# Optimization experiments

Hardware: AMD Instinct MI355X
Metric: run time of the kernel (lower is better)

## Reference

```python
import jax, jax.numpy as jnp
import numpy as np

# Dims: B nodes, Z species (elements), IN/OUT channels, M = 2*l+1 (l=1)
B, Z, IN, OUT, M = 8192, 10, 512, 512, 3
ALPHA = 1.0 / np.sqrt(IN)  # self.alpha = 1/sqrt(in_dim)
SQRT3 = float(np.sqrt(3.0))


def setup_inputs() -> dict:
    key = jax.random.key(0)
    k1, k2, k3 = jax.random.split(key, 3)
    t = jax.random.normal(k1, (B, IN, M), dtype=jnp.float32)
    species = jax.random.randint(k2, (B,), 0, Z)
    node_attrs = jax.nn.one_hot(species, Z, dtype=jnp.float32)  # [B, Z] one-hot
    # torch.nn.init.uniform_(weights, -sqrt(3), sqrt(3))
    weights = jax.random.uniform(k3, (Z, OUT, IN), dtype=jnp.float32,
                                 minval=-SQRT3, maxval=SQRT3)
    return {"t": t, "node_attrs": node_attrs, "weights": weights}


def reference(t, node_attrs, weights):
    # Faithful to: einsum('bz, zCc, bcd -> bCd', node_attrs, weights*alpha, t)
    # Contract weights with t first per species ([Z,B,C,M], ~500MB), which
    # avoids the huge [B,C,c] per-node weight-gather intermediate, then
    # select/sum over species with the one-hot node_attrs.
    W = weights * ALPHA                       # [Z, OUT, IN]
    zt = jnp.einsum('zCc,bcd->zbCd', W, t)    # [Z, B, OUT, M]
    out = jnp.einsum('bz,zbCd->bCd', node_attrs, zt)  # [B, OUT, M]
    return out
```

## Files before the change

### kernel.cpp

```cpp
#include <hip/hip_runtime.h>
#include <stdint.h>

#define NB   8192
#define NZ   10
#define CIN  512
#define COUT 512
#define MM   3
#define ALPHA 0.04419417382415922f

#define ROWS_TOTAL (NB * MM)
#define BM 128
#define BN 128
#define BK 32
#define KITERS (CIN / BK)
#define MAX_MT (ROWS_TOTAL / BM + NZ)
#define NYB (COUT / BN)
#define NWG (MAX_MT * NYB)
#define NGRP 32

typedef short bf16x8 __attribute__((ext_vector_type(8)));
typedef float f32x4  __attribute__((ext_vector_type(4)));

__device__ __forceinline__ uint16_t f2bf(float f) {
    union { float f; uint32_t i; } v; v.f = f;
    uint32_t x = v.i;
    x += 0x7fffu + ((x >> 16) & 1u);
    return (uint16_t)(x >> 16);
}
__device__ __forceinline__ uint32_t pack2(float a, float b) {
    return (uint32_t)f2bf(a) | ((uint32_t)f2bf(b) << 16);
}
__device__ __forceinline__ void async16(const void* g, void* l) {
    __builtin_amdgcn_global_load_lds((const uint32_t*)g, (uint32_t*)l, 16, 0, 0);
}

__global__ __launch_bounds__(256)
void prep_kernel(const float* __restrict__ attrs, const float* __restrict__ w,
                 int* __restrict__ species, int* __restrict__ hist,
                 ushort* __restrict__ wt) {
    const int tid = threadIdx.x;
    if (blockIdx.x >= NGRP) {
        const size_t base = (size_t)(blockIdx.x - NGRP) * 2048;
        const float* src = w + base;
        ushort* dst = wt + base;
        float4 a = *(const float4*)(src + tid * 4);
        float4 b = *(const float4*)(src + 1024 + tid * 4);
        uint2 oa, ob;
        oa.x = pack2(a.x, a.y); oa.y = pack2(a.z, a.w);
        ob.x = pack2(b.x, b.y); ob.y = pack2(b.z, b.w);
        *(uint2*)(dst + tid * 4) = oa;
        *(uint2*)(dst + 1024 + tid * 4) = ob;
        return;
    }
    __shared__ int wc[4][NZ];
    const int b = blockIdx.x * 256 + tid;
    const float* a = attrs + (size_t)b * NZ;
    int s = 0;
    #pragma unroll
    for (int z = 0; z < NZ; z++) if (a[z] > 0.5f) s = z;
    species[b] = s;
    const int wv = tid >> 6, lane = tid & 63;
    #pragma unroll
    for (int z = 0; z < NZ; z++) {
        unsigned long long m = __ballot(s == z);
        if (lane == 0) wc[wv][z] = __popcll(m);
    }
    __syncthreads();
    if (tid < NZ) {
        hist[blockIdx.x * NZ + tid] = wc[0][tid] + wc[1][tid] + wc[2][tid] + wc[3][tid];
    }
}

__global__ __launch_bounds__(256)
void place_kernel(const int* __restrict__ species, const int* __restrict__ hist,
                  int* __restrict__ sorted, int* __restrict__ offsets,
                  int* __restrict__ tile_offsets) {
    __shared__ int lhist[NGRP][NZ];
    __shared__ int loff[NZ + 1], ltoff[NZ + 1];
    __shared__ int pb[NZ];
    __shared__ int wc[4][NZ];
    const int tid = threadIdx.x, g = blockIdx.x;

    for (int i = tid; i < NGRP * NZ; i += 256) ((int*)lhist)[i] = hist[i];
    __syncthreads();
    if (tid == 0) {
        int off = 0, toff = 0;
        for (int z = 0; z < NZ; z++) {
            int tot = 0;
            for (int gg = 0; gg < NGRP; gg++) tot += lhist[gg][z];
            loff[z] = off; ltoff[z] = toff;
            off += tot;
            toff += (3 * tot + BM - 1) / BM;
        }
        loff[NZ] = off; ltoff[NZ] = toff;
    }
    __syncthreads();
    if (tid < NZ) {
        int base = loff[tid];
        for (int gg = 0; gg < g; gg++) base += lhist[gg][tid];
        pb[tid] = base;
    }
    if (g == 0 && tid < NZ + 1) {
        offsets[tid] = loff[tid];
        tile_offsets[tid] = ltoff[tid];
    }
    const int b = g * 256 + tid;
    const int s = species[b];
    const int wv = tid >> 6, lane = tid & 63;
    unsigned long long mymask = 0;
    #pragma unroll
    for (int z = 0; z < NZ; z++) {
        unsigned long long m = __ballot(s == z);
        if (lane == 0) wc[wv][z] = __popcll(m);
        if (s == z) mymask = m;
    }
    __syncthreads();
    int rank = __popcll(mymask & ((1ull << lane) - 1ull));
    #pragma unroll
    for (int w2 = 0; w2 < 4; w2++) if (w2 < wv) rank += wc[w2][s];
    sorted[pb[s] + rank] = b;
}

__global__ __launch_bounds__(256)
void pack_t(const float* __restrict__ t, const int* __restrict__ sorted,
            ushort* __restrict__ tt) {
    const int w = threadIdx.x >> 6, L = threadIdx.x & 63;
    const int p = blockIdx.x * 4 + w;
    const int node = sorted[p];
    const float4* src = (const float4*)(t + (size_t)node * (CIN * MM) + L * 24);
    float4 f[6];
    #pragma unroll
    for (int i = 0; i < 6; i++) f[i] = src[i];
    const float* v = (const float*)f;
    #pragma unroll
    for (int d = 0; d < MM; d++) {
        uint4 o;
        o.x = pack2(v[d],      v[3 + d]);
        o.y = pack2(v[6 + d],  v[9 + d]);
        o.z = pack2(v[12 + d], v[15 + d]);
        o.w = pack2(v[18 + d], v[21 + d]);
        *(uint4*)&tt[(size_t)(3 * p + d) * CIN + L * 8] = o;
    }
}

__global__ __launch_bounds__(256)
void gemm_kernel(const ushort* __restrict__ tt, const ushort* __restrict__ wt,
                 const int* __restrict__ sorted, const int* __restrict__ offsets,
                 const int* __restrict__ tile_offsets, float* __restrict__ out) {
    __shared__ __align__(16) ushort smem[2][2][BM][BK];
    __shared__ int spos[48];

    const int bid = blockIdx.x;
    const int nid = (bid & 7) * (NWG / 8) + (bid >> 3);
    const int tz = nid >> 2;
    const int Cbase = (nid & 3) * BN;

    if (tz >= tile_offsets[NZ]) return;
    int z = 0;
    #pragma unroll
    for (int i = 1; i < NZ; i++) if (tile_offsets[i] <= tz) z = i;

    const int row_base = 3 * offsets[z] + (tz - tile_offsets[z]) * BM;
    const int row_end  = 3 * offsets[z + 1];
    const int pos0     = row_base / 3;

    const int tid = threadIdx.x;
    const int w = tid >> 6, L = tid & 63;
    if (tid < 48) spos[tid] = sorted[min(pos0 + tid, NB - 1)];

    const int lr = L >> 2;
    const int cs = (L & 3) ^ ((L >> 3) & 3);
    const int soff = lr * CIN + cs * 8;
    const ushort* gA = tt + (size_t)(row_base + w * 32) * CIN + soff;
    const ushort* gB = wt + ((size_t)z * COUT + Cbase + w * 32) * CIN + soff;

    const int wm = w & 1, wn = w >> 1;
    const int q = L >> 4, mr = L & 15;
    const int sr8 = (q ^ ((mr >> 1) & 3)) * 8;

    f32x4 acc[4][4];
    #pragma unroll
    for (int i = 0; i < 4; i++)
        #pragma unroll
        for (int j = 0; j < 4; j++) acc[i][j] = (f32x4){0.f, 0.f, 0.f, 0.f};

#define STAGE(bufi, ko) do {                                        \
        async16(gA + (ko),                  &smem[0][bufi][w * 32][0]);      \
        async16(gA + 16 * CIN + (ko),       &smem[0][bufi][w * 32 + 16][0]); \
        async16(gB + (ko),                  &smem[1][bufi][w * 32][0]);      \
        async16(gB + 16 * CIN + (ko),       &smem[1][bufi][w * 32 + 16][0]); \
    } while (0)

    STAGE(0, 0);
    for (int kt = 0; kt < KITERS; kt++) {
        const int cur = kt & 1;
        if (kt + 1 < KITERS) {
            STAGE(cur ^ 1, (kt + 1) * BK);
            asm volatile("s_waitcnt vmcnt(4)" ::: "memory");
        } else {
            asm volatile("s_waitcnt vmcnt(0)" ::: "memory");
        }
        asm volatile("s_barrier" ::: "memory");

        bf16x8 af[4], bf[4];
        #pragma unroll
        for (int am = 0; am < 4; am++)
            af[am] = *(const bf16x8*)&smem[0][cur][wm * 64 + am * 16 + mr][sr8];
        #pragma unroll
        for (int bn = 0; bn < 4; bn++)
            bf[bn] = *(const bf16x8*)&smem[1][cur][wn * 64 + bn * 16 + mr][sr8];
        #pragma unroll
        for (int am = 0; am < 4; am++)
            #pragma unroll
            for (int bn = 0; bn < 4; bn++)
                acc[am][bn] = __builtin_amdgcn_mfma_f32_16x16x32_bf16(
                    af[am], bf[bn], acc[am][bn], 0, 0, 0);

        asm volatile("s_barrier" ::: "memory");
    }
#undef STAGE

    float* ebuf = (float*)smem;
    #pragma unroll
    for (int ch = 0; ch < 3; ch++) {
        __syncthreads();
        const int pbase = pos0 + ch * 16;
        #pragma unroll
        for (int am = 0; am < 4; am++) {
            #pragma unroll
            for (int r = 0; r < 4; r++) {
                const int Rg = row_base + wm * 64 + am * 16 + q * 4 + r;
                const int pos = Rg / 3;
                const int d = Rg - 3 * pos;
                const int lp = pos - pbase;
                if (lp >= 0 && lp < 16 && Rg < row_end) {
                    #pragma unroll
                    for (int bn = 0; bn < 4; bn++) {
                        const int c = wn * 64 + bn * 16 + mr;
                        ebuf[(lp * BN + c) * 3 + d] = ALPHA * acc[am][bn][r];
                    }
                }
            }
        }
        __syncthreads();
        #pragma unroll 4
        for (int j = 0; j < 24; j++) {
            const int idx = j * 256 + tid;
            const int lp  = idx / 384;
            const int o   = idx - lp * 384;
            const int pos = pbase + lp;
            const int d   = o % 3;
            const int row = 3 * pos + d;
            if (row >= row_base && row < row_base + BM && row < row_end) {
                const int node = spos[pos - pos0];
                out[(size_t)node * (COUT * MM) + Cbase * 3 + o] = ebuf[idx];
            }
        }
    }
}

extern "C" void kernel_launch(void* const* d_in, const int* in_sizes, int n_in,
                              void* d_out, int out_size, void* d_ws, size_t ws_size,
                              hipStream_t stream) {
    const float* t     = (const float*)d_in[0];
    const float* attrs = (const float*)d_in[1];
    const float* w     = (const float*)d_in[2];
    float* out = (float*)d_out;

    uint8_t* ws = (uint8_t*)d_ws;
    int* species      = (int*)ws;                  ws += NB * 4;
    int* sorted       = (int*)ws;                  ws += NB * 4;
    int* hist         = (int*)ws;                  ws += NGRP * NZ * 4;
    int* offsets      = (int*)ws;                  ws += 16 * 4;
    int* tile_offsets = (int*)ws;                  ws += 16 * 4;
    ws = (uint8_t*)(((uintptr_t)ws + 255) & ~(uintptr_t)255);
    ushort* wt = (ushort*)ws;                      ws += (size_t)NZ * COUT * CIN * 2;
    ushort* tt = (ushort*)ws;

    hipLaunchKernelGGL(prep_kernel, dim3(NGRP + (NZ * COUT * CIN) / 2048), dim3(256),
                       0, stream, attrs, w, species, hist, wt);
    hipLaunchKernelGGL(place_kernel, dim3(NGRP), dim3(256), 0, stream,
                       species, hist, sorted, offsets, tile_offsets);
    hipLaunchKernelGGL(pack_t, dim3(NB / 4), dim3(256), 0, stream, t, sorted, tt);
    hipLaunchKernelGGL(gemm_kernel, dim3(NWG), dim3(256), 0, stream,
                       tt, wt, sorted, offsets, tile_offsets, out);
}
```

Baseline: 152.7 us.

## Enlarge GEMM tiles to 256x256 with triple-buffered split A/B staging

Doubles the GEMM block tile to 256x256 with 512 threads, so each wave computes a 128x64 sub-tile and loads from the A and B operands are reused more. The shared-memory ring grows from two to three stages in dynamic LDS, with A and B prefetch issued at different barriers and MFMA sections raised in priority with setprio. Workgroups are remapped across the eight XCDs for the new grid size, and the scatter epilogue is widened to the bigger tile. In exchange the grid shrinks to about 212 workgroups, which leaves part of the CUs idle, and register and LDS pressure per workgroup go up.

```diff
diff --git a/kernel.cpp b/kernel.cpp
--- a/kernel.cpp
+++ b/kernel.cpp
@@ -9,10 +9,10 @@
 #define ALPHA 0.04419417382415922f
 
 #define ROWS_TOTAL (NB * MM)
-#define BM 128
-#define BN 128
+#define BM 256
+#define BN 256
 #define BK 32
-#define KITERS (CIN / BK)
+#define NKT (CIN / BK)
 #define MAX_MT (ROWS_TOTAL / BM + NZ)
 #define NYB (COUT / BN)
 #define NWG (MAX_MT * NYB)
@@ -143,17 +143,18 @@
     }
 }
 
-__global__ __launch_bounds__(256)
+__global__ __launch_bounds__(512, 2)
 void gemm_kernel(const ushort* __restrict__ tt, const ushort* __restrict__ wt,
                  const int* __restrict__ sorted, const int* __restrict__ offsets,
                  const int* __restrict__ tile_offsets, float* __restrict__ out) {
-    __shared__ __align__(16) ushort smem[2][2][BM][BK];
-    __shared__ int spos[48];
+    extern __shared__ __align__(16) ushort smem[];
+    __shared__ int spos[96];
 
     const int bid = blockIdx.x;
-    const int nid = (bid & 7) * (NWG / 8) + (bid >> 3);
-    const int tz = nid >> 2;
-    const int Cbase = (nid & 3) * BN;
+    const int xcd = bid & 7, ii = bid >> 3;
+    const int wg = (xcd < 4 ? xcd * 27 : 108 + (xcd - 4) * 26) + ii;
+    const int tz = wg >> 1;
+    const int Cbase = (wg & 1) * BN;
 
     if (tz >= tile_offsets[NZ]) return;
     int z = 0;
@@ -166,70 +167,97 @@
 
     const int tid = threadIdx.x;
     const int w = tid >> 6, L = tid & 63;
-    if (tid < 48) spos[tid] = sorted[min(pos0 + tid, NB - 1)];
-
-    const int lr = L >> 2;
-    const int cs = (L & 3) ^ ((L >> 3) & 3);
-    const int soff = lr * CIN + cs * 8;
-    const ushort* gA = tt + (size_t)(row_base + w * 32) * CIN + soff;
-    const ushort* gB = wt + ((size_t)z * COUT + Cbase + w * 32) * CIN + soff;
+    if (tid < 96) spos[tid] = sorted[min(pos0 + tid, NB - 1)];
+
+    const int lr16 = w * 16 + (L >> 2);
+    const int cs   = (L & 3) ^ ((L >> 3) & 3);
+    const size_t aoff = (size_t)(row_base + lr16) * CIN + cs * 8;
+    const size_t boff = ((size_t)z * COUT + Cbase + lr16) * CIN + cs * 8;
+
+#define ASLOT(s) (smem + (s) * 16384)
+#define BSLOT(s) (smem + (s) * 16384 + 8192)
+#define STAGE_A(s, kt) do {                                                  \
+        async16(tt + aoff + (kt) * BK,                    ASLOT(s) + w * 512);          \
+        async16(tt + aoff + (size_t)128 * CIN + (kt) * BK, ASLOT(s) + 4096 + w * 512);  \
+    } while (0)
+#define STAGE_B(s, kt) do {                                                  \
+        async16(wt + boff + (kt) * BK,                    BSLOT(s) + w * 512);          \
+        async16(wt + boff + (size_t)128 * CIN + (kt) * BK, BSLOT(s) + 4096 + w * 512);  \
+    } while (0)
 
     const int wm = w & 1, wn = w >> 1;
     const int q = L >> 4, mr = L & 15;
-    const int sr8 = (q ^ ((mr >> 1) & 3)) * 8;
-
-    f32x4 acc[4][4];
-    #pragma unroll
-    for (int i = 0; i < 4; i++)
+    const int qs = (q ^ ((mr >> 1) & 3)) * 8;
+
+    f32x4 acc[8][4];
+    #pragma unroll
+    for (int i = 0; i < 8; i++)
         #pragma unroll
         for (int j = 0; j < 4; j++) acc[i][j] = (f32x4){0.f, 0.f, 0.f, 0.f};
 
-#define STAGE(bufi, ko) do {                                        \
-        async16(gA + (ko),                  &smem[0][bufi][w * 32][0]);      \
-        async16(gA + 16 * CIN + (ko),       &smem[0][bufi][w * 32 + 16][0]); \
-        async16(gB + (ko),                  &smem[1][bufi][w * 32][0]);      \
-        async16(gB + 16 * CIN + (ko),       &smem[1][bufi][w * 32 + 16][0]); \
-    } while (0)
-
-    STAGE(0, 0);
-    for (int kt = 0; kt < KITERS; kt++) {
-        const int cur = kt & 1;
-        if (kt + 1 < KITERS) {
-            STAGE(cur ^ 1, (kt + 1) * BK);
+    STAGE_A(0, 0); STAGE_B(0, 0);
+    STAGE_A(1, 1); STAGE_B(1, 1);
+
+    int cur = 0, stg = 2;
+    for (int kt = 0; kt < NKT; kt++) {
+        if (kt + 1 < NKT) {
             asm volatile("s_waitcnt vmcnt(4)" ::: "memory");
         } else {
             asm volatile("s_waitcnt vmcnt(0)" ::: "memory");
         }
         asm volatile("s_barrier" ::: "memory");
-
+        if (kt + 2 < NKT) STAGE_A(stg, kt + 2);
+
+        const ushort* Ab = ASLOT(cur);
+        const ushort* Bb = BSLOT(cur);
         bf16x8 af[4], bf[4];
         #pragma unroll
         for (int am = 0; am < 4; am++)
-            af[am] = *(const bf16x8*)&smem[0][cur][wm * 64 + am * 16 + mr][sr8];
+            af[am] = *(const bf16x8*)(Ab + (wm * 128 + am * 16 + mr) * 32 + qs);
         #pragma unroll
         for (int bn = 0; bn < 4; bn++)
-            bf[bn] = *(const bf16x8*)&smem[1][cur][wn * 64 + bn * 16 + mr][sr8];
+            bf[bn] = *(const bf16x8*)(Bb + (wn * 64 + bn * 16 + mr) * 32 + qs);
+        __builtin_amdgcn_s_setprio(1);
         #pragma unroll
         for (int am = 0; am < 4; am++)
             #pragma unroll
             for (int bn = 0; bn < 4; bn++)
                 acc[am][bn] = __builtin_amdgcn_mfma_f32_16x16x32_bf16(
                     af[am], bf[bn], acc[am][bn], 0, 0, 0);
+        __builtin_amdgcn_s_setprio(0);
 
         asm volatile("s_barrier" ::: "memory");
-    }
-#undef STAGE
+        if (kt + 2 < NKT) STAGE_B(stg, kt + 2);
+
+        bf16x8 ag[4];
+        #pragma unroll
+        for (int am = 0; am < 4; am++)
+            ag[am] = *(const bf16x8*)(Ab + (wm * 128 + (am + 4) * 16 + mr) * 32 + qs);
+        __builtin_amdgcn_s_setprio(1);
+        #pragma unroll
+        for (int am = 0; am < 4; am++)
+            #pragma unroll
+            for (int bn = 0; bn < 4; bn++)
+                acc[am + 4][bn] = __builtin_amdgcn_mfma_f32_16x16x32_bf16(
+                    ag[am], bf[bn], acc[am + 4][bn], 0, 0, 0);
+        __builtin_amdgcn_s_setprio(0);
+
+        cur = (cur == 2) ? 0 : cur + 1;
+        stg = (stg == 2) ? 0 : stg + 1;
+    }
+#undef STAGE_A
+#undef STAGE_B
 
     float* ebuf = (float*)smem;
     #pragma unroll
-    for (int ch = 0; ch < 3; ch++) {
+    for (int ch = 0; ch < 6; ch++) {
         __syncthreads();
         const int pbase = pos0 + ch * 16;
         #pragma unroll
-        for (int am = 0; am < 4; am++) {
+        for (int am = 0; am < 8; am++) {
             #pragma unroll
             for (int r = 0; r < 4; r++) {
-                const int Rg = row_base + wm * 64 + am * 16 + q * 4 + r;
+                const int Rg = row_base + wm * 128 + am * 16 + q * 4 + r;
                 const int pos = Rg / 3;
                 const int d = Rg - 3 * pos;
                 const int lp = pos - pbase;
@@ -245,9 +273,9 @@
         __syncthreads();
         #pragma unroll 4
         for (int j = 0; j < 24; j++) {
-            const int idx = j * 256 + tid;
-            const int lp  = idx / 384;
-            const int o   = idx - lp * 384;
+            const int idx = j * 512 + tid;
+            const int lp  = idx / 768;
+            const int o   = idx - lp * 768;
             const int pos = pbase + lp;
             const int d   = o % 3;
             const int row = 3 * pos + d;
@@ -282,6 +310,6 @@
     hipLaunchKernelGGL(place_kernel, dim3(NGRP), dim3(256), 0, stream,
                        species, hist, sorted, offsets, tile_offsets);
     hipLaunchKernelGGL(pack_t, dim3(NB / 4), dim3(256), 0, stream, t, sorted, tt);
-    hipLaunchKernelGGL(gemm_kernel, dim3(NWG), dim3(256), 0, stream,
+    hipLaunchKernelGGL(gemm_kernel, dim3(NWG), dim3(512), 3 * 2 * 256 * BK * 2, stream,
                        tt, wt, sorted, offsets, tile_offsets, out);
 }
```

Measured after the change: 149.9 us. About the same (-1.9%).
